# Kernel tuning notes

Measured on AMD Instinct MI355X. Metric: run time of the kernel, lower is better.

## Reference

```python
import jax, jax.numpy as jnp
import numpy as np

N = 100000        # num nodes
E2 = 3200000      # num directed edges (symmetric)
D = 256           # node feature dim
C = 40            # num classes
NIDS = 1000       # labelled node ids
TOL = 0.01
MAXITER = 16
AVG_DEG = E2 // N // 2 * 2  # ~32


def setup_inputs() -> dict:
    key = jax.random.key(0)
    k1, k2, k3, k4, k5, k6 = jax.random.split(key, 6)
    E = E2 // 2
    row_h = jax.random.randint(k1, (E,), 0, N, dtype=jnp.int32)
    col_h = jax.random.randint(k2, (E,), 0, N, dtype=jnp.int32)
    # symmetrize so I - (1-eps)*A is SPD-like (CG assumption)
    row = jnp.concatenate([row_h, col_h])
    col = jnp.concatenate([col_h, row_h])
    vals = jax.random.uniform(k3, (E,), dtype=jnp.float32) * (0.9 / 32.0)
    data = jnp.concatenate([vals, vals])
    node_features = jax.random.normal(k4, (N, D), dtype=jnp.float32)
    ids = jax.random.randint(k5, (NIDS,), 0, N, dtype=jnp.int32)
    # hk.Linear with TruncatedNormal(stddev=1/sqrt(D)) init
    W = (jax.random.truncated_normal(k6, -2.0, 2.0, (D, C), dtype=jnp.float32)
         * (1.0 / np.sqrt(D))).astype(jnp.float32)
    b = jnp.zeros((C,), jnp.float32)
    e0 = jnp.zeros((), jnp.float32)  # hk.get_parameter('e0', (), init=zeros)
    return dict(node_features=node_features, W=W, b=b, e0=e0,
                data=data, row=row, col=col, ids=ids)


def reference(node_features, W, b, e0, data, row, col, ids):
    epsilon = jax.nn.sigmoid(e0)
    # head_transform=None; d_feat > num_classes -> Linear first, then smooth
    x = node_features @ W + b  # [N, C]

    def spmv(v):  # adj @ v for COO adjacency, v: [N, C]
        return jax.ops.segment_sum(data[:, None] * v[col], row, num_segments=N)

    def f(v):  # (I - (1-eps) A) v
        return v - (1.0 - epsilon) * spmv(v)

    # smooth(): x.shape[1] (=C) <= ids.size -> direct CG on dense x, then gather ids
    sol, _ = jax.scipy.sparse.linalg.cg(f, x, tol=TOL, maxiter=MAXITER)
    return sol[ids]  # [NIDS, C] logits
```

## Files before the change

kernel.cpp:

```cpp
#include <hip/hip_runtime.h>
#include <hip/hip_fp16.h>
#include <math.h>

#define NNODE  100000
#define NEDGE  3200000
#define DFEAT  256
#define NCLS   40
#define NC_TOT 4000000
#define NIDS   1000
#define TOLSQ  1.0e-4f
#define MAXIT  16

#define SB 2048
#define SLOT_TOT 1000000
#define SPB 489
#define XB 1024
#define VT 256
#define GR     128
#define GKC    32
#define GEMM_B 782

#define RB      128
#define NBUCK   782
#define BCAP    6144
#define SUBB    1024
#define NPB     800
#define EPB     4000

__device__ __forceinline__ float block_reduce_256(float v, float* red) {
  int tid = threadIdx.x;
  red[tid] = v;
  __syncthreads();
  #pragma unroll
  for (int off = 128; off > 0; off >>= 1) {
    if (tid < off) red[tid] += red[tid + off];
    __syncthreads();
  }
  float res = red[0];
  __syncthreads();
  return res;
}

__global__ void __launch_bounds__(256) k_pcount(const int* __restrict__ row,
                                                int* __restrict__ cntmat,
                                                int* __restrict__ total) {
  __shared__ int h[NBUCK];
  int tid = threadIdx.x, blk = blockIdx.x;
  for (int i = tid; i < NBUCK; i += 256) h[i] = 0;
  __syncthreads();
  int e0 = blk * EPB;
  for (int i = tid; i < EPB; i += 256) atomicAdd(&h[row[e0 + i] >> 7], 1);
  __syncthreads();
  for (int i = tid; i < NBUCK; i += 256) {
    int v = h[i];
    cntmat[blk * NBUCK + i] = v;
    if (v) atomicAdd(&total[i], v);
  }
}

__global__ void k_bscan2(const int* __restrict__ total, int* __restrict__ bptr) {
  __shared__ int s[1024];
  int tid = threadIdx.x;
  int v = (tid < NBUCK) ? total[tid] : 0;
  s[tid] = v;
  __syncthreads();
  for (int off = 1; off < 1024; off <<= 1) {
    int t = (tid >= off) ? s[tid - off] : 0;
    __syncthreads();
    s[tid] += t;
    __syncthreads();
  }
  if (tid < NBUCK) bptr[tid] = s[tid] - v;
  if (tid == 0) bptr[NBUCK] = NEDGE;
}

__global__ void __launch_bounds__(1024) k_colscan(int* __restrict__ cntmat,
                                                  const int* __restrict__ bptr) {
  __shared__ int s[1024];
  int b = blockIdx.x;
  int tid = threadIdx.x;
  int v = (tid < NPB) ? cntmat[tid * NBUCK + b] : 0;
  s[tid] = v;
  __syncthreads();
  for (int off = 1; off < 1024; off <<= 1) {
    int t = (tid >= off) ? s[tid - off] : 0;
    __syncthreads();
    s[tid] += t;
    __syncthreads();
  }
  if (tid < NPB) cntmat[tid * NBUCK + b] = bptr[b] + s[tid] - v;
}

__global__ void __launch_bounds__(256) k_ppart(const int* __restrict__ row,
    const int* __restrict__ col, const float* __restrict__ data,
    const int* __restrict__ offmat, uint2* __restrict__ bstage) {
  __shared__ int cnt[NBUCK];
  __shared__ int segs[NBUCK + 1];
  __shared__ int cur[NBUCK];
  __shared__ int goff[NBUCK];
  __shared__ int scp[256];
  __shared__ unsigned short bof[EPB];
  __shared__ uint2 pay[EPB];
  int tid = threadIdx.x, blk = blockIdx.x;
  int e0 = blk * EPB;

  for (int i = tid; i < NBUCK; i += 256) {
    cnt[i] = 0;
    goff[i] = offmat[blk * NBUCK + i];
  }
  __syncthreads();
  for (int i = tid; i < EPB; i += 256) atomicAdd(&cnt[row[e0 + i] >> 7], 1);
  __syncthreads();

  int t4 = tid * 4;
  int l0 = (t4 + 0 < NBUCK) ? cnt[t4 + 0] : 0;
  int l1 = (t4 + 1 < NBUCK) ? cnt[t4 + 1] : 0;
  int l2 = (t4 + 2 < NBUCK) ? cnt[t4 + 2] : 0;
  int l3 = (t4 + 3 < NBUCK) ? cnt[t4 + 3] : 0;
  int mysum = l0 + l1 + l2 + l3;
  scp[tid] = mysum;
  __syncthreads();
  for (int off = 1; off < 256; off <<= 1) {
    int t = (tid >= off) ? scp[tid - off] : 0;
    __syncthreads();
    scp[tid] += t;
    __syncthreads();
  }
  int base = scp[tid] - mysum;
  if (t4 + 0 <= NBUCK) segs[t4 + 0] = base;  base += l0;
  if (t4 + 1 <= NBUCK) segs[t4 + 1] = base;  base += l1;
  if (t4 + 2 <= NBUCK) segs[t4 + 2] = base;  base += l2;
  if (t4 + 3 <= NBUCK) segs[t4 + 3] = base;
  for (int i = tid; i < NBUCK; i += 256) cur[i] = 0;
  __syncthreads();

  for (int b = tid; b < NBUCK; b += 256) {
    int s1 = segs[b + 1];
    for (int i = segs[b]; i < s1; ++i) bof[i] = (unsigned short)b;
  }
  for (int i = tid; i < EPB; i += 256) {
    int rr = row[e0 + i];
    int b = rr >> 7;
    int rk = atomicAdd(&cur[b], 1);
    pay[segs[b] + rk] = make_uint2(((unsigned)(rr & (RB - 1)) << 17) | (unsigned)col[e0 + i],
                                   __float_as_uint(data[e0 + i]));
  }
  __syncthreads();
  for (int i = tid; i < EPB; i += 256) {
    int b = bof[i];
    bstage[goff[b] + (i - segs[b])] = pay[i];
  }
}

__global__ void __launch_bounds__(256) k_bbuild(const int* __restrict__ bptr,
    const uint2* __restrict__ bstage, int* __restrict__ rowptr,
    int2* __restrict__ csr) {
  __shared__ uint2 ebuf[BCAP];
  __shared__ int deg[SUBB];
  __shared__ int segs[SUBB];
  __shared__ int scp[256];
  int b = blockIdx.x;
  int s0 = bptr[b], s1 = bptr[b + 1];
  int n = s1 - s0;
  if (n > BCAP) n = BCAP;
  int tid = threadIdx.x;
  for (int i = tid; i < SUBB; i += 256) deg[i] = 0;
  __syncthreads();
  for (int i = tid; i < n; i += 256) {
    uint2 e = bstage[s0 + i];
    ebuf[i] = e;
    int key = (int)(e.x >> 17) * 8 + (int)((e.x & 0x1FFFF) >> 14);
    atomicAdd(&deg[key], 1);
  }
  __syncthreads();
  int t4 = tid * 4;
  int l0 = deg[t4 + 0], l1 = deg[t4 + 1], l2 = deg[t4 + 2], l3 = deg[t4 + 3];
  int mysum = l0 + l1 + l2 + l3;
  scp[tid] = mysum;
  __syncthreads();
  for (int off = 1; off < 256; off <<= 1) {
    int t = (tid >= off) ? scp[tid - off] : 0;
    __syncthreads();
    scp[tid] += t;
    __syncthreads();
  }
  int base = scp[tid] - mysum;
  segs[t4 + 0] = base;  base += l0;
  segs[t4 + 1] = base;  base += l1;
  segs[t4 + 2] = base;  base += l2;
  segs[t4 + 3] = base;
  __syncthreads();
  for (int i = tid; i < SUBB; i += 256) deg[i] = 0;
  if (tid < RB) {
    int grow = b * RB + tid;
    if (grow < NNODE) rowptr[grow] = s0 + segs[tid * 8];
  }
  if (b == 0 && tid == 0) rowptr[NNODE] = NEDGE;
  __syncthreads();
  for (int i = tid; i < n; i += 256) {
    uint2 e = ebuf[i];
    int col = (int)(e.x & 0x1FFFF);
    int key = (int)(e.x >> 17) * 8 + (col >> 14);
    int pos = atomicAdd(&deg[key], 1);
    csr[s0 + segs[key] + pos] = make_int2(col, (int)e.y);
  }
}

__global__ void __launch_bounds__(256) k_gemm(const float* __restrict__ feat,
    const float* __restrict__ W, const float* __restrict__ bias,
    float* __restrict__ r, float* __restrict__ p, __half* __restrict__ ph,
    float* __restrict__ part) {
  __shared__ float ftile[GR][GKC + 1];
  __shared__ float wtile[GKC * NCLS];
  __shared__ float red[256];
  int tid = threadIdx.x;
  int r0 = blockIdx.x * GR;
  int rl0 = (tid >> 2) * 2;
  int cbase = (tid & 3) * 10;
  float acc0[10], acc1[10];
  #pragma unroll
  for (int j = 0; j < 10; ++j) {
    float bv = bias[cbase + j];
    acc0[j] = bv;
    acc1[j] = bv;
  }

  for (int k0 = 0; k0 < DFEAT; k0 += GKC) {
    __syncthreads();
    #pragma unroll
    for (int it = 0; it < 4; ++it) {
      int i = tid + it * 256;
      int rr = i >> 3, kq = i & 7;
      int grow = r0 + rr;
      float4 v = make_float4(0.f, 0.f, 0.f, 0.f);
      if (grow < NNODE)
        v = *(const float4*)(feat + (size_t)grow * DFEAT + k0 + kq * 4);
      ftile[rr][kq * 4 + 0] = v.x;
      ftile[rr][kq * 4 + 1] = v.y;
      ftile[rr][kq * 4 + 2] = v.z;
      ftile[rr][kq * 4 + 3] = v.w;
    }
    #pragma unroll
    for (int it = 0; it < 5; ++it) {
      int i = tid + it * 256;
      wtile[i] = W[k0 * NCLS + i];
    }
    __syncthreads();
    #pragma unroll 4
    for (int kk = 0; kk < GKC; ++kk) {
      float f0 = ftile[rl0][kk];
      float f1 = ftile[rl0 + 1][kk];
      const float* wr = &wtile[kk * NCLS + cbase];
      #pragma unroll
      for (int j = 0; j < 10; ++j) {
        float w = wr[j];
        acc0[j] = fmaf(f0, w, acc0[j]);
        acc1[j] = fmaf(f1, w, acc1[j]);
      }
    }
  }

  float local = 0.f;
  int g0 = r0 + rl0, g1 = g0 + 1;
  if (g0 < NNODE) {
    size_t b0 = (size_t)g0 * NCLS + cbase;
    #pragma unroll
    for (int j = 0; j < 10; ++j) {
      float a = acc0[j];
      r[b0 + j] = a; p[b0 + j] = a; ph[b0 + j] = __float2half(a);
      local = fmaf(a, a, local);
    }
  }
  if (g1 < NNODE) {
    size_t b1 = (size_t)g1 * NCLS + cbase;
    #pragma unroll
    for (int j = 0; j < 10; ++j) {
      float a = acc1[j];
      r[b1 + j] = a; p[b1 + j] = a; ph[b1 + j] = __float2half(a);
      local = fmaf(a, a, local);
    }
  }
  float tot = block_reduce_256(local, red);
  if (tid == 0) part[blockIdx.x] = tot;
}

__global__ void k_init_scal(const float* __restrict__ part, const float* __restrict__ e0,
                            float* __restrict__ scal) {
  __shared__ float red[256];
  float local = 0.f;
  for (int i = threadIdx.x; i < GEMM_B; i += 256) local += part[i];
  float bs = block_reduce_256(local, red);
  if (threadIdx.x == 0) {
    float eps = 1.f / (1.f + expf(-e0[0]));
    scal[0] = 1.f - eps;
    scal[1] = TOLSQ * bs;
    scal[2] = bs;
  }
}

__global__ void __launch_bounds__(VT) k_spmv(const float* __restrict__ scal, int k,
    const int* __restrict__ rowptr, const int2* __restrict__ csr,
    const __half* __restrict__ ph, const float* __restrict__ p,
    float* __restrict__ Ap, float* __restrict__ part) {
  float gamma = scal[2 + k], atol2 = scal[1];
  if (!(gamma > atol2)) return;
  float omega = scal[0];
  int b = blockIdx.x;
  int chunk = (b & 7) * (SB / 8) + (b >> 3);
  int sbase = chunk * SPB;
  float local = 0.f;
  #pragma unroll
  for (int it = 0; it < 2; ++it) {
    int li = threadIdx.x + it * VT;
    int s = sbase + li;
    if (li < SPB && s < SLOT_TOT) {
      int rr = s / 10;
      int cq4 = (s - rr * 10) * 4;
      int s0 = rowptr[rr], s1 = rowptr[rr + 1];
      float a0 = 0.f, a1 = 0.f, a2 = 0.f, a3 = 0.f;
      #pragma unroll 4
      for (int j = s0; j < s1; ++j) {
        int2 pr = csr[j];
        float w = __int_as_float(pr.y);
        uint2 g = *(const uint2*)(ph + (size_t)pr.x * NCLS + cq4);
        __half2 h01 = *(__half2*)&g.x;
        __half2 h23 = *(__half2*)&g.y;
        float2 f01 = __half22float2(h01);
        float2 f23 = __half22float2(h23);
        a0 = fmaf(w, f01.x, a0);
        a1 = fmaf(w, f01.y, a1);
        a2 = fmaf(w, f23.x, a2);
        a3 = fmaf(w, f23.y, a3);
      }
      size_t e = (size_t)rr * NCLS + cq4;
      float4 pe = *(const float4*)(p + e);
      float4 v;
      v.x = fmaf(-omega, a0, pe.x);
      v.y = fmaf(-omega, a1, pe.y);
      v.z = fmaf(-omega, a2, pe.z);
      v.w = fmaf(-omega, a3, pe.w);
      *(float4*)(Ap + e) = v;
      local = fmaf(pe.x, v.x, local);
      local = fmaf(pe.y, v.y, local);
      local = fmaf(pe.z, v.z, local);
      local = fmaf(pe.w, v.w, local);
    }
  }
  __shared__ float red[256];
  float tot = block_reduce_256(local, red);
  if (threadIdx.x == 0) part[blockIdx.x] = tot;
}

__global__ void __launch_bounds__(VT) k_xr(const float* __restrict__ scal, int k,
    const float* __restrict__ part_in,
    const float* __restrict__ p, const float* __restrict__ Ap,
    float* __restrict__ r, const int* __restrict__ ids,
    float* __restrict__ out, float* __restrict__ part_out) {
  float gamma = scal[2 + k], atol2 = scal[1];
  if (!(gamma > atol2)) return;
  __shared__ float red[256];
  float lp = 0.f;
  for (int i = threadIdx.x; i < SB; i += VT) lp += part_in[i];
  float pap = block_reduce_256(lp, red);
  float alpha = gamma / pap;
  int idx = blockIdx.x * VT + threadIdx.x;
  if (idx < NIDS * NCLS) {
    int i = idx / NCLS, c = idx - (idx / NCLS) * NCLS;
    out[idx] += alpha * p[(size_t)ids[i] * NCLS + c];
  }
  const float4* a4 = (const float4*)Ap;
  float4* r4 = (float4*)r;
  float local = 0.f;
  int stride = gridDim.x * blockDim.x;
  for (int e = blockIdx.x * blockDim.x + threadIdx.x; e < NC_TOT / 4; e += stride) {
    float4 ae = a4[e], re = r4[e];
    re.x = fmaf(-alpha, ae.x, re.x); re.y = fmaf(-alpha, ae.y, re.y);
    re.z = fmaf(-alpha, ae.z, re.z); re.w = fmaf(-alpha, ae.w, re.w);
    r4[e] = re;
    local = fmaf(re.x, re.x, local); local = fmaf(re.y, re.y, local);
    local = fmaf(re.z, re.z, local); local = fmaf(re.w, re.w, local);
  }
  float tot = block_reduce_256(local, red);
  if (threadIdx.x == 0) part_out[blockIdx.x] = tot;
}

__global__ void __launch_bounds__(VT) k_pupd(float* __restrict__ scal, int k,
    const float* __restrict__ part_in,
    const float* __restrict__ r, float* __restrict__ p, __half* __restrict__ ph) {
  float gamma = scal[2 + k], atol2 = scal[1];
  if (!(gamma > atol2)) {
    if (blockIdx.x == 0 && threadIdx.x == 0) scal[2 + k + 1] = gamma;
    return;
  }
  __shared__ float red[256];
  float lp = 0.f;
  for (int i = threadIdx.x; i < XB; i += VT) lp += part_in[i];
  float gnew = block_reduce_256(lp, red);
  float beta = gnew / gamma;
  const float4* r4 = (const float4*)r;
  float4* p4 = (float4*)p;
  int stride = gridDim.x * blockDim.x;
  for (int e = blockIdx.x * blockDim.x + threadIdx.x; e < NC_TOT / 4; e += stride) {
    float4 pe = p4[e], re = r4[e];
    pe.x = fmaf(beta, pe.x, re.x); pe.y = fmaf(beta, pe.y, re.y);
    pe.z = fmaf(beta, pe.z, re.z); pe.w = fmaf(beta, pe.w, re.w);
    p4[e] = pe;
    int e4 = e * 4;
    ph[e4 + 0] = __float2half(pe.x);
    ph[e4 + 1] = __float2half(pe.y);
    ph[e4 + 2] = __float2half(pe.z);
    ph[e4 + 3] = __float2half(pe.w);
  }
  if (blockIdx.x == 0 && threadIdx.x == 0) scal[2 + k + 1] = gnew;
}

extern "C" void kernel_launch(void* const* d_in, const int* in_sizes, int n_in,
                              void* d_out, int out_size, void* d_ws, size_t ws_size,
                              hipStream_t stream) {
  const float* feat = (const float*)d_in[0];
  const float* W    = (const float*)d_in[1];
  const float* bias = (const float*)d_in[2];
  const float* e0   = (const float*)d_in[3];
  const float* data = (const float*)d_in[4];
  const int*   row  = (const int*)d_in[5];
  const int*   col  = (const int*)d_in[6];
  const int*   ids  = (const int*)d_in[7];
  float* out = (float*)d_out;

  size_t off = 0;
  char* base = (char*)d_ws;
  auto take = [&](size_t nbytes) -> void* {
    void* ptr = base + off;
    off += (nbytes + 255) & ~(size_t)255;
    return ptr;
  };
  float* rv  = (float*)take((size_t)NC_TOT * 4);
  float* pv  = (float*)take((size_t)NC_TOT * 4);
  float* ap  = (float*)take((size_t)NC_TOT * 4);
  __half* ph = (__half*)take((size_t)NC_TOT * 2);
  int2*  csr = (int2*)take((size_t)NEDGE * 8);
  int* rowptr    = (int*)take((size_t)(NNODE + 1) * 4);
  int* cntmat    = (int*)take((size_t)NPB * NBUCK * 4);
  int* total     = (int*)take((size_t)(NBUCK + 2) * 4);
  int* bptr      = (int*)take((size_t)(NBUCK + 2) * 4);
  float* part_a  = (float*)take(SB * 4);
  float* part_b  = (float*)take(XB * 4);
  float* scal    = (float*)take(64 * 4);

  uint2* bstage = (uint2*)rv;

  hipMemsetAsync(total, 0, (size_t)(NBUCK + 2) * 4, stream);
  hipMemsetAsync(out, 0, (size_t)NIDS * NCLS * 4, stream);
  k_pcount<<<NPB, 256, 0, stream>>>(row, cntmat, total);
  k_bscan2<<<1, 1024, 0, stream>>>(total, bptr);
  k_colscan<<<NBUCK, 1024, 0, stream>>>(cntmat, bptr);
  k_ppart<<<NPB, 256, 0, stream>>>(row, col, data, cntmat, bstage);
  k_bbuild<<<NBUCK, 256, 0, stream>>>(bptr, bstage, rowptr, csr);

  k_gemm<<<GEMM_B, 256, 0, stream>>>(feat, W, bias, rv, pv, ph, part_a);
  k_init_scal<<<1, 256, 0, stream>>>(part_a, e0, scal);

  for (int k = 0; k < MAXIT; ++k) {
    k_spmv<<<SB, VT, 0, stream>>>(scal, k, rowptr, csr, ph, pv, ap, part_a);
    k_xr  <<<XB, VT, 0, stream>>>(scal, k, part_a, pv, ap, rv, ids, out, part_b);
    k_pupd<<<XB, VT, 0, stream>>>(scal, k, part_b, rv, pv, ph);
  }
}
```

Measured before the change: 422.2 us.

## Fuse CG iterations into one persistent cooperative kernel with grid syncs

Replaces the per-iteration trio of SpMV, residual-update and direction-update launches, plus the scalar-init kernel, with a single cooperative persistent kernel. Grid-wide synchronisation separates the phases, and the CG scalars (omega, tolerance, gamma) stay in registers instead of a global scal array. This removes about 48 kernel launches and the early-exit checks each launch made. In exchange the grid size is capped by occupancy, which may reduce parallelism for the irregular SpMV phase, and grid.sync adds its own overhead.

New measurement: 1.064 ms. 152% more time.

```diff
diff --git a/kernel.cpp b/kernel.cpp
--- a/kernel.cpp
+++ b/kernel.cpp
@@ -1,6 +1,9 @@
 #include <hip/hip_runtime.h>
 #include <hip/hip_fp16.h>
+#include <hip/hip_cooperative_groups.h>
 #include <math.h>
+
+namespace cg = cooperative_groups;
 
 #define NNODE  100000
 #define NEDGE  3200000
@@ -11,10 +14,7 @@
 #define TOLSQ  1.0e-4f
 #define MAXIT  16
 
-#define SB 2048
 #define SLOT_TOT 1000000
-#define SPB 489
-#define XB 1024
 #define VT 256
 #define GR     128
 #define GKC    32
@@ -284,134 +284,119 @@
   if (tid == 0) part[blockIdx.x] = tot;
 }
 
-__global__ void k_init_scal(const float* __restrict__ part, const float* __restrict__ e0,
-                            float* __restrict__ scal) {
+__global__ void __launch_bounds__(256) k_cg(
+    const int* __restrict__ rowptr, const int2* __restrict__ csr,
+    __half* __restrict__ ph, float* __restrict__ p, float* __restrict__ Ap,
+    float* __restrict__ r, const int* __restrict__ ids,
+    float* __restrict__ out, const float* __restrict__ part_g,
+    const float* __restrict__ e0, float* __restrict__ part_a,
+    float* __restrict__ part_b) {
+  cg::grid_group grid = cg::this_grid();
   __shared__ float red[256];
-  float local = 0.f;
-  for (int i = threadIdx.x; i < GEMM_B; i += 256) local += part[i];
-  float bs = block_reduce_256(local, red);
-  if (threadIdx.x == 0) {
-    float eps = 1.f / (1.f + expf(-e0[0]));
-    scal[0] = 1.f - eps;
-    scal[1] = TOLSQ * bs;
-    scal[2] = bs;
-  }
-}
-
-__global__ void __launch_bounds__(VT) k_spmv(const float* __restrict__ scal, int k,
-    const int* __restrict__ rowptr, const int2* __restrict__ csr,
-    const __half* __restrict__ ph, const float* __restrict__ p,
-    float* __restrict__ Ap, float* __restrict__ part) {
-  float gamma = scal[2 + k], atol2 = scal[1];
-  if (!(gamma > atol2)) return;
-  float omega = scal[0];
-  int b = blockIdx.x;
-  int chunk = (b & 7) * (SB / 8) + (b >> 3);
-  int sbase = chunk * SPB;
-  float local = 0.f;
-  #pragma unroll
-  for (int it = 0; it < 2; ++it) {
-    int li = threadIdx.x + it * VT;
-    int s = sbase + li;
-    if (li < SPB && s < SLOT_TOT) {
-      int rr = s / 10;
-      int cq4 = (s - rr * 10) * 4;
-      int s0 = rowptr[rr], s1 = rowptr[rr + 1];
-      float a0 = 0.f, a1 = 0.f, a2 = 0.f, a3 = 0.f;
-      #pragma unroll 4
-      for (int j = s0; j < s1; ++j) {
-        int2 pr = csr[j];
-        float w = __int_as_float(pr.y);
-        uint2 g = *(const uint2*)(ph + (size_t)pr.x * NCLS + cq4);
-        __half2 h01 = *(__half2*)&g.x;
-        __half2 h23 = *(__half2*)&g.y;
-        float2 f01 = __half22float2(h01);
-        float2 f23 = __half22float2(h23);
-        a0 = fmaf(w, f01.x, a0);
-        a1 = fmaf(w, f01.y, a1);
-        a2 = fmaf(w, f23.x, a2);
-        a3 = fmaf(w, f23.y, a3);
+  const int tid = threadIdx.x, b = blockIdx.x, nb = gridDim.x;
+
+  float lp = 0.f;
+  for (int i = tid; i < GEMM_B; i += VT) lp += part_g[i];
+  float bs = block_reduce_256(lp, red);
+  float eps = 1.f / (1.f + expf(-e0[0]));
+  const float omega = 1.f - eps;
+  const float atol2 = TOLSQ * bs;
+  float gamma = bs;
+
+  const int spb = (SLOT_TOT + nb - 1) / nb;
+  const int chunk = (b & 7) * (nb >> 3) + (b >> 3);
+  const int sbase = chunk * spb;
+  const int gstride = nb * VT;
+
+  for (int k = 0; k < MAXIT && gamma > atol2; ++k) {
+    float local = 0.f;
+    for (int li = tid; li < spb; li += VT) {
+      int s = sbase + li;
+      if (s < SLOT_TOT) {
+        int rr_ = s / 10;
+        int cq4 = (s - rr_ * 10) * 4;
+        int s0 = rowptr[rr_], s1 = rowptr[rr_ + 1];
+        float a0 = 0.f, a1 = 0.f, a2 = 0.f, a3 = 0.f;
+        #pragma unroll 4
+        for (int j = s0; j < s1; ++j) {
+          int2 pr = csr[j];
+          float w = __int_as_float(pr.y);
+          uint2 g = *(const uint2*)(ph + (size_t)pr.x * NCLS + cq4);
+          __half2 h01 = *(__half2*)&g.x;
+          __half2 h23 = *(__half2*)&g.y;
+          float2 f01 = __half22float2(h01);
+          float2 f23 = __half22float2(h23);
+          a0 = fmaf(w, f01.x, a0);
+          a1 = fmaf(w, f01.y, a1);
+          a2 = fmaf(w, f23.x, a2);
+          a3 = fmaf(w, f23.y, a3);
+        }
+        size_t e = (size_t)rr_ * NCLS + cq4;
+        float4 pe = *(const float4*)(p + e);
+        float4 v;
+        v.x = fmaf(-omega, a0, pe.x);
+        v.y = fmaf(-omega, a1, pe.y);
+        v.z = fmaf(-omega, a2, pe.z);
+        v.w = fmaf(-omega, a3, pe.w);
+        *(float4*)(Ap + e) = v;
+        local = fmaf(pe.x, v.x, local);
+        local = fmaf(pe.y, v.y, local);
+        local = fmaf(pe.z, v.z, local);
+        local = fmaf(pe.w, v.w, local);
       }
-      size_t e = (size_t)rr * NCLS + cq4;
-      float4 pe = *(const float4*)(p + e);
-      float4 v;
-      v.x = fmaf(-omega, a0, pe.x);
-      v.y = fmaf(-omega, a1, pe.y);
-      v.z = fmaf(-omega, a2, pe.z);
-      v.w = fmaf(-omega, a3, pe.w);
-      *(float4*)(Ap + e) = v;
-      local = fmaf(pe.x, v.x, local);
-      local = fmaf(pe.y, v.y, local);
-      local = fmaf(pe.z, v.z, local);
-      local = fmaf(pe.w, v.w, local);
-    }
-  }
-  __shared__ float red[256];
-  float tot = block_reduce_256(local, red);
-  if (threadIdx.x == 0) part[blockIdx.x] = tot;
-}
-
-__global__ void __launch_bounds__(VT) k_xr(const float* __restrict__ scal, int k,
-    const float* __restrict__ part_in,
-    const float* __restrict__ p, const float* __restrict__ Ap,
-    float* __restrict__ r, const int* __restrict__ ids,
-    float* __restrict__ out, float* __restrict__ part_out) {
-  float gamma = scal[2 + k], atol2 = scal[1];
-  if (!(gamma > atol2)) return;
-  __shared__ float red[256];
-  float lp = 0.f;
-  for (int i = threadIdx.x; i < SB; i += VT) lp += part_in[i];
-  float pap = block_reduce_256(lp, red);
-  float alpha = gamma / pap;
-  int idx = blockIdx.x * VT + threadIdx.x;
-  if (idx < NIDS * NCLS) {
-    int i = idx / NCLS, c = idx - (idx / NCLS) * NCLS;
-    out[idx] += alpha * p[(size_t)ids[i] * NCLS + c];
-  }
-  const float4* a4 = (const float4*)Ap;
-  float4* r4 = (float4*)r;
-  float local = 0.f;
-  int stride = gridDim.x * blockDim.x;
-  for (int e = blockIdx.x * blockDim.x + threadIdx.x; e < NC_TOT / 4; e += stride) {
-    float4 ae = a4[e], re = r4[e];
-    re.x = fmaf(-alpha, ae.x, re.x); re.y = fmaf(-alpha, ae.y, re.y);
-    re.z = fmaf(-alpha, ae.z, re.z); re.w = fmaf(-alpha, ae.w, re.w);
-    r4[e] = re;
-    local = fmaf(re.x, re.x, local); local = fmaf(re.y, re.y, local);
-    local = fmaf(re.z, re.z, local); local = fmaf(re.w, re.w, local);
-  }
-  float tot = block_reduce_256(local, red);
-  if (threadIdx.x == 0) part_out[blockIdx.x] = tot;
-}
-
-__global__ void __launch_bounds__(VT) k_pupd(float* __restrict__ scal, int k,
-    const float* __restrict__ part_in,
-    const float* __restrict__ r, float* __restrict__ p, __half* __restrict__ ph) {
-  float gamma = scal[2 + k], atol2 = scal[1];
-  if (!(gamma > atol2)) {
-    if (blockIdx.x == 0 && threadIdx.x == 0) scal[2 + k + 1] = gamma;
-    return;
-  }
-  __shared__ float red[256];
-  float lp = 0.f;
-  for (int i = threadIdx.x; i < XB; i += VT) lp += part_in[i];
-  float gnew = block_reduce_256(lp, red);
-  float beta = gnew / gamma;
-  const float4* r4 = (const float4*)r;
-  float4* p4 = (float4*)p;
-  int stride = gridDim.x * blockDim.x;
-  for (int e = blockIdx.x * blockDim.x + threadIdx.x; e < NC_TOT / 4; e += stride) {
-    float4 pe = p4[e], re = r4[e];
-    pe.x = fmaf(beta, pe.x, re.x); pe.y = fmaf(beta, pe.y, re.y);
-    pe.z = fmaf(beta, pe.z, re.z); pe.w = fmaf(beta, pe.w, re.w);
-    p4[e] = pe;
-    int e4 = e * 4;
-    ph[e4 + 0] = __float2half(pe.x);
-    ph[e4 + 1] = __float2half(pe.y);
-    ph[e4 + 2] = __float2half(pe.z);
-    ph[e4 + 3] = __float2half(pe.w);
-  }
-  if (blockIdx.x == 0 && threadIdx.x == 0) scal[2 + k + 1] = gnew;
+    }
+    float tot = block_reduce_256(local, red);
+    if (tid == 0) part_a[b] = tot;
+    grid.sync();
+
+    lp = 0.f;
+    for (int i = tid; i < nb; i += VT) lp += part_a[i];
+    float pap = block_reduce_256(lp, red);
+    float alpha = gamma / pap;
+    int idx = b * VT + tid;
+    if (idx < NIDS * NCLS) {
+      int i = idx / NCLS, c = idx - (idx / NCLS) * NCLS;
+      out[idx] += alpha * p[(size_t)ids[i] * NCLS + c];
+    }
+    local = 0.f;
+    {
+      const float4* a4 = (const float4*)Ap;
+      float4* r4 = (float4*)r;
+      for (int e = b * VT + tid; e < NC_TOT / 4; e += gstride) {
+        float4 ae = a4[e], re = r4[e];
+        re.x = fmaf(-alpha, ae.x, re.x); re.y = fmaf(-alpha, ae.y, re.y);
+        re.z = fmaf(-alpha, ae.z, re.z); re.w = fmaf(-alpha, ae.w, re.w);
+        r4[e] = re;
+        local = fmaf(re.x, re.x, local); local = fmaf(re.y, re.y, local);
+        local = fmaf(re.z, re.z, local); local = fmaf(re.w, re.w, local);
+      }
+    }
+    tot = block_reduce_256(local, red);
+    if (tid == 0) part_b[b] = tot;
+    grid.sync();
+
+    lp = 0.f;
+    for (int i = tid; i < nb; i += VT) lp += part_b[i];
+    float gnew = block_reduce_256(lp, red);
+    float beta = gnew / gamma;
+    {
+      const float4* r4 = (const float4*)r;
+      float4* p4 = (float4*)p;
+      for (int e = b * VT + tid; e < NC_TOT / 4; e += gstride) {
+        float4 pe = p4[e], re = r4[e];
+        pe.x = fmaf(beta, pe.x, re.x); pe.y = fmaf(beta, pe.y, re.y);
+        pe.z = fmaf(beta, pe.z, re.z); pe.w = fmaf(beta, pe.w, re.w);
+        p4[e] = pe;
+        int e4 = e * 4;
+        ph[e4 + 0] = __float2half(pe.x);
+        ph[e4 + 1] = __float2half(pe.y);
+        ph[e4 + 2] = __float2half(pe.z);
+        ph[e4 + 3] = __float2half(pe.w);
+      }
+    }
+    gamma = gnew;
+    grid.sync();
+  }
 }
 
 extern "C" void kernel_launch(void* const* d_in, const int* in_sizes, int n_in,
@@ -443,9 +428,9 @@
   int* cntmat    = (int*)take((size_t)NPB * NBUCK * 4);
   int* total     = (int*)take((size_t)(NBUCK + 2) * 4);
   int* bptr      = (int*)take((size_t)(NBUCK + 2) * 4);
-  float* part_a  = (float*)take(SB * 4);
-  float* part_b  = (float*)take(XB * 4);
-  float* scal    = (float*)take(64 * 4);
+  float* part_g  = (float*)take(2048 * 4);
+  float* part_a  = (float*)take(2048 * 4);
+  float* part_b  = (float*)take(2048 * 4);
 
   uint2* bstage = (uint2*)rv;
 
@@ -457,12 +442,18 @@
   k_ppart<<<NPB, 256, 0, stream>>>(row, col, data, cntmat, bstage);
   k_bbuild<<<NBUCK, 256, 0, stream>>>(bptr, bstage, rowptr, csr);
 
-  k_gemm<<<GEMM_B, 256, 0, stream>>>(feat, W, bias, rv, pv, ph, part_a);
-  k_init_scal<<<1, 256, 0, stream>>>(part_a, e0, scal);
-
-  for (int k = 0; k < MAXIT; ++k) {
-    k_spmv<<<SB, VT, 0, stream>>>(scal, k, rowptr, csr, ph, pv, ap, part_a);
-    k_xr  <<<XB, VT, 0, stream>>>(scal, k, part_a, pv, ap, rv, ids, out, part_b);
-    k_pupd<<<XB, VT, 0, stream>>>(scal, k, part_b, rv, pv, ph);
-  }
-}
+  k_gemm<<<GEMM_B, 256, 0, stream>>>(feat, W, bias, rv, pv, ph, part_g);
+
+  int occ = 0;
+  hipOccupancyMaxActiveBlocksPerMultiprocessor(&occ, (const void*)k_cg, VT, 0);
+  if (occ < 1) occ = 1;
+  int nb = occ * 256;
+  if (nb > 2048) nb = 2048;
+  nb &= ~7;
+  if (nb < 256) nb = 256;
+
+  void* args[] = {(void*)&rowptr, (void*)&csr, (void*)&ph, (void*)&pv,
+                  (void*)&ap, (void*)&rv, (void*)&ids, (void*)&out,
+                  (void*)&part_g, (void*)&e0, (void*)&part_a, (void*)&part_b};
+  hipLaunchCooperativeKernel((const void*)k_cg, dim3(nb), dim3(VT), args, 0, stream);
+}
```
